# Kernel optimization log

Measured on AMD Instinct MI355X. Metric: run time of the kernel, lower is better.

The kernel has to match this reference:

```python
import jax, jax.numpy as jnp
import numpy as np

DIM = 192
K = 3
RED = 4
B, H, W = 4, 256, 256
EPS = 1e-5  # BatchNorm eps

def _make_mask():
    # PixelCNN mask type 'A': zero the center pixel and everything after it
    m = np.ones((DIM, 1, K, K), np.float32)
    m[:, :, K // 2, K // 2:] = 0.0  # center row: center col onward
    m[:, :, K // 2 + 1:] = 0.0      # all rows below center
    return jnp.asarray(m)

MASK = _make_mask()  # [DIM, 1, K, K]

def setup_inputs() -> dict:
    key = jax.random.key(0)
    ks = jax.random.split(key, 4)
    r = DIM // RED
    return {
        "x": jax.random.normal(ks[0], (B, DIM, H, W), jnp.float32),
        "w1": jax.random.normal(ks[1], (r, DIM), jnp.float32) * 0.05,      # conv1 1x1, no bias
        "gamma": jnp.ones((r,), jnp.float32),                               # BN weight
        "beta": jnp.zeros((r,), jnp.float32),                               # BN bias
        "running_mean": jnp.zeros((r,), jnp.float32),
        "running_var": jnp.ones((r,), jnp.float32),
        "w2": jax.random.normal(ks[2], (DIM * K * K, r), jnp.float32) * 0.05,  # conv2 1x1
        "b2": jnp.zeros((DIM * K * K,), jnp.float32),
        "bias": jnp.zeros((DIM,), jnp.float32),                             # depthwise conv bias
    }

def reference(x, w1, gamma, beta, running_mean, running_var, w2, b2, bias):
    b, c, h, w = x.shape  # c == DIM
    # --- dynamic weight generation: pool -> 1x1 conv -> BN(eval) -> ReLU -> 1x1 conv ---
    pooled = x.mean(axis=(2, 3))                                   # [b, dim]
    t = pooled @ w1.T                                              # [b, dim//red]
    t = gamma * (t - running_mean) * jax.lax.rsqrt(running_var + EPS) + beta
    t = jax.nn.relu(t)
    wt = t @ w2.T + b2                                             # [b, dim*K*K]
    wt = wt.reshape(b * DIM, 1, K, K) * jnp.tile(MASK, (b, 1, 1, 1))
    # --- per-sample masked depthwise conv via batch-folding (groups = b*dim) ---
    out = jax.lax.conv_general_dilated(
        x.reshape(1, b * c, h, w), wt,
        window_strides=(1, 1), padding=((1, 1), (1, 1)),
        feature_group_count=b * DIM,
        dimension_numbers=("NCHW", "OIHW", "NCHW"))                # [1, b*dim, h, w]
    out = out + jnp.tile(bias, (b,))[None, :, None, None]
    return out.reshape(b, c, h, w)
```

## Files before the change

kernel.cpp:

```cpp
#include <hip/hip_runtime.h>

#define DIMC 192
#define HID  48
#define HW   65536
#define WIDTH 256
#define NPLANE 768

__global__ __launch_bounds__(1024) void k_pool(const float* __restrict__ x,
                                               float* __restrict__ pooled) {
    const int plane = blockIdx.x;
    const float4* p = (const float4*)(x + (size_t)plane * HW);
    const int t = threadIdx.x;
    float s = 0.f;
#pragma unroll
    for (int k = 0; k < 16; ++k) {
        float4 v = p[k * 1024 + t];
        s += (v.x + v.y) + (v.z + v.w);
    }
#pragma unroll
    for (int off = 32; off > 0; off >>= 1) s += __shfl_down(s, off, 64);
    __shared__ float wsum[16];
    const int wave = t >> 6, lane = t & 63;
    if (lane == 0) wsum[wave] = s;
    __syncthreads();
    if (t == 0) {
        float tot = 0.f;
#pragma unroll
        for (int i = 0; i < 16; ++i) tot += wsum[i];
        pooled[plane] = tot * (1.0f / 65536.0f);
    }
}

__global__ __launch_bounds__(256) void k_weights(
    const float* __restrict__ pooled,
    const float* __restrict__ w1,
    const float* __restrict__ gamma,
    const float* __restrict__ beta,
    const float* __restrict__ rmean,
    const float* __restrict__ rvar,
    const float* __restrict__ w2,
    const float* __restrict__ b2,
    float* __restrict__ w4)
{
    const int b = blockIdx.x;
    const int tid = threadIdx.x;
    __shared__ float P[DIMC];
    __shared__ float T[HID];
    if (tid < DIMC) P[tid] = pooled[b * DIMC + tid];
    __syncthreads();
    if (tid < HID) {
        const float* wr = w1 + tid * DIMC;
        float acc = 0.f;
        for (int d = 0; d < DIMC; ++d) acc += P[d] * wr[d];
        const float inv = 1.0f / sqrtf(rvar[tid] + 1e-5f);
        float v = gamma[tid] * (acc - rmean[tid]) * inv + beta[tid];
        T[tid] = v > 0.f ? v : 0.f;
    }
    __syncthreads();
    for (int idx = tid; idx < DIMC * 4; idx += 256) {
        const int c = idx >> 2, tap = idx & 3;
        const int o = c * 9 + tap;
        const float* wr = w2 + o * HID;
        float acc = b2[o];
        for (int j = 0; j < HID; ++j) acc += T[j] * wr[j];
        w4[b * DIMC * 4 + idx] = acc;
    }
}

__global__ __launch_bounds__(256) void k_conv(const float* __restrict__ x,
                                              const float4* __restrict__ w4,
                                              const float* __restrict__ bias,
                                              float* __restrict__ out) {
    const int plane = blockIdx.x >> 3;
    const int c = plane % DIMC;
    const int wave = threadIdx.x >> 6;
    const int lane = threadIdx.x & 63;
    const int y0 = ((blockIdx.x & 7) << 5) + (wave << 3);
    const float4 wt = w4[plane];
    const float bs = bias[c];
    const float4* xp = (const float4*)(x + (size_t)plane * HW);
    float4* op = (float4*)(out + (size_t)plane * HW);

    float4 a;
    if (y0 == 0) a = make_float4(0.f, 0.f, 0.f, 0.f);
    else         a = xp[(y0 - 1) * 64 + lane];

#pragma unroll
    for (int r = 0; r < 8; ++r) {
        const int y = y0 + r;
        float4 bb = xp[y * 64 + lane];
        float leftA  = __shfl_up(a.w, 1, 64);   if (lane == 0)  leftA  = 0.f;
        float rightA = __shfl_down(a.x, 1, 64); if (lane == 63) rightA = 0.f;
        float leftB  = __shfl_up(bb.w, 1, 64);  if (lane == 0)  leftB  = 0.f;
        float4 o;
        o.x = wt.x * leftA + wt.y * a.x + wt.z * a.y   + wt.w * leftB + bs;
        o.y = wt.x * a.x   + wt.y * a.y + wt.z * a.z   + wt.w * bb.x  + bs;
        o.z = wt.x * a.y   + wt.y * a.z + wt.z * a.w   + wt.w * bb.y  + bs;
        o.w = wt.x * a.z   + wt.y * a.w + wt.z * rightA + wt.w * bb.z + bs;
        op[y * 64 + lane] = o;
        a = bb;
    }
}

extern "C" void kernel_launch(void* const* d_in, const int* in_sizes, int n_in,
                              void* d_out, int out_size, void* d_ws, size_t ws_size,
                              hipStream_t stream) {
    const float* x     = (const float*)d_in[0];
    const float* w1    = (const float*)d_in[1];
    const float* gamma = (const float*)d_in[2];
    const float* beta  = (const float*)d_in[3];
    const float* rmean = (const float*)d_in[4];
    const float* rvar  = (const float*)d_in[5];
    const float* w2    = (const float*)d_in[6];
    const float* b2    = (const float*)d_in[7];
    const float* bias  = (const float*)d_in[8];
    float* out = (float*)d_out;

    float* pooled = (float*)d_ws;
    float* w4     = pooled + NPLANE;

    k_pool<<<NPLANE, 1024, 0, stream>>>(x, pooled);
    k_weights<<<4, 256, 0, stream>>>(pooled, w1, gamma, beta, rmean, rvar, w2, b2, w4);
    k_conv<<<NPLANE * 8, 256, 0, stream>>>(x, (const float4*)w4, bias, out);
}
```

Baseline: 392.7 us.

## Fuse dynamic weight generation into conv kernel and use nontemporal output stores

Removes the separate weight-generation kernel launch. Each conv block now recomputes the hidden MLP layer for its sample and the four unmasked taps for its channel, with a shuffle-reduced dot product. Output stores become nontemporal so the write stream does not pollute cache. This drops one launch and one serialization point, but every block redundantly computes a 48x192 matvec before starting the convolution.

```diff
diff --git a/kernel.cpp b/kernel.cpp
--- a/kernel.cpp
+++ b/kernel.cpp
@@ -5,6 +5,8 @@
 #define HW   65536
 #define WIDTH 256
 #define NPLANE 768
+
+typedef float nfloat4 __attribute__((ext_vector_type(4)));
 
 __global__ __launch_bounds__(1024) void k_pool(const float* __restrict__ x,
                                                float* __restrict__ pooled) {
@@ -31,7 +33,8 @@
     }
 }
 
-__global__ __launch_bounds__(256) void k_weights(
+__global__ __launch_bounds__(256) void k_conv(
+    const float* __restrict__ x,
     const float* __restrict__ pooled,
     const float* __restrict__ w1,
     const float* __restrict__ gamma,
@@ -40,46 +43,51 @@
     const float* __restrict__ rvar,
     const float* __restrict__ w2,
     const float* __restrict__ b2,
-    float* __restrict__ w4)
+    const float* __restrict__ bias,
+    float* __restrict__ out)
 {
-    const int b = blockIdx.x;
+    const int plane = blockIdx.x >> 3;
+    const int b = plane / DIMC;
+    const int c = plane - b * DIMC;
     const int tid = threadIdx.x;
-    __shared__ float P[DIMC];
+
     __shared__ float T[HID];
-    if (tid < DIMC) P[tid] = pooled[b * DIMC + tid];
-    __syncthreads();
-    if (tid < HID) {
-        const float* wr = w1 + tid * DIMC;
-        float acc = 0.f;
-        for (int d = 0; d < DIMC; ++d) acc += P[d] * wr[d];
-        const float inv = 1.0f / sqrtf(rvar[tid] + 1e-5f);
-        float v = gamma[tid] * (acc - rmean[tid]) * inv + beta[tid];
-        T[tid] = v > 0.f ? v : 0.f;
+    __shared__ float W4[4];
+    {
+        const int g = tid >> 2, l = tid & 3;
+        if (g < HID) {
+            const float* pr = pooled + b * DIMC;
+            const float* wr = w1 + g * DIMC;
+            float acc = 0.f;
+#pragma unroll 8
+            for (int d = l; d < DIMC; d += 4) acc += pr[d] * wr[d];
+            acc += __shfl_xor(acc, 1, 64);
+            acc += __shfl_xor(acc, 2, 64);
+            if (l == 0) {
+                const float inv = rsqrtf(rvar[g] + 1e-5f);
+                float v = gamma[g] * (acc - rmean[g]) * inv + beta[g];
+                T[g] = v > 0.f ? v : 0.f;
+            }
+        }
+        __syncthreads();
+        if (tid < 4) {
+            const int o = c * 9 + tid;
+            const float* wr = w2 + o * HID;
+            float acc = b2[o];
+#pragma unroll
+            for (int j = 0; j < HID; ++j) acc += T[j] * wr[j];
+            W4[tid] = acc;
+        }
+        __syncthreads();
     }
-    __syncthreads();
-    for (int idx = tid; idx < DIMC * 4; idx += 256) {
-        const int c = idx >> 2, tap = idx & 3;
-        const int o = c * 9 + tap;
-        const float* wr = w2 + o * HID;
-        float acc = b2[o];
-        for (int j = 0; j < HID; ++j) acc += T[j] * wr[j];
-        w4[b * DIMC * 4 + idx] = acc;
-    }
-}
+    const float4 wt = make_float4(W4[0], W4[1], W4[2], W4[3]);
+    const float bs = bias[c];
 
-__global__ __launch_bounds__(256) void k_conv(const float* __restrict__ x,
-                                              const float4* __restrict__ w4,
-                                              const float* __restrict__ bias,
-                                              float* __restrict__ out) {
-    const int plane = blockIdx.x >> 3;
-    const int c = plane % DIMC;
-    const int wave = threadIdx.x >> 6;
-    const int lane = threadIdx.x & 63;
+    const int wave = tid >> 6;
+    const int lane = tid & 63;
     const int y0 = ((blockIdx.x & 7) << 5) + (wave << 3);
-    const float4 wt = w4[plane];
-    const float bs = bias[c];
     const float4* xp = (const float4*)(x + (size_t)plane * HW);
-    float4* op = (float4*)(out + (size_t)plane * HW);
+    nfloat4* op = (nfloat4*)(out + (size_t)plane * HW);
 
     float4 a;
     if (y0 == 0) a = make_float4(0.f, 0.f, 0.f, 0.f);
@@ -92,12 +100,12 @@
         float leftA  = __shfl_up(a.w, 1, 64);   if (lane == 0)  leftA  = 0.f;
         float rightA = __shfl_down(a.x, 1, 64); if (lane == 63) rightA = 0.f;
         float leftB  = __shfl_up(bb.w, 1, 64);  if (lane == 0)  leftB  = 0.f;
-        float4 o;
-        o.x = wt.x * leftA + wt.y * a.x + wt.z * a.y   + wt.w * leftB + bs;
-        o.y = wt.x * a.x   + wt.y * a.y + wt.z * a.z   + wt.w * bb.x  + bs;
-        o.z = wt.x * a.y   + wt.y * a.z + wt.z * a.w   + wt.w * bb.y  + bs;
-        o.w = wt.x * a.z   + wt.y * a.w + wt.z * rightA + wt.w * bb.z + bs;
-        op[y * 64 + lane] = o;
+        nfloat4 o;
+        o.x = wt.x * leftA + wt.y * a.x + wt.z * a.y    + wt.w * leftB + bs;
+        o.y = wt.x * a.x   + wt.y * a.y + wt.z * a.z    + wt.w * bb.x  + bs;
+        o.z = wt.x * a.y   + wt.y * a.z + wt.z * a.w    + wt.w * bb.y  + bs;
+        o.w = wt.x * a.z   + wt.y * a.w + wt.z * rightA + wt.w * bb.z  + bs;
+        __builtin_nontemporal_store(o, &op[y * 64 + lane]);
         a = bb;
     }
 }
@@ -117,9 +125,8 @@
     float* out = (float*)d_out;
 
     float* pooled = (float*)d_ws;
-    float* w4     = pooled + NPLANE;
 
     k_pool<<<NPLANE, 1024, 0, stream>>>(x, pooled);
-    k_weights<<<4, 256, 0, stream>>>(pooled, w1, gamma, beta, rmean, rvar, w2, b2, w4);
-    k_conv<<<NPLANE * 8, 256, 0, stream>>>(x, (const float4*)w4, bias, out);
+    k_conv<<<NPLANE * 8, 256, 0, stream>>>(x, pooled, w1, gamma, beta,
+                                           rmean, rvar, w2, b2, bias, out);
 }
```

New measurement: 382.4 us. 2.6% less time.
